# Kernel tuning notes

Hardware: AMD Instinct MI355X
Metric: run time of the kernel (lower is better)

The kernel has to match this reference:

```python
import jax, jax.numpy as jnp
import numpy as np

B, N, F, H, OUT = 64, 512, 128, 256, 6


def setup_inputs() -> dict:
    key = jax.random.key(0)
    ks = jax.random.split(key, 20)
    s = 0.02
    inp = {
        "x": jax.random.normal(ks[0], (B * N, F), dtype=jnp.float32),
        "edge_index": jax.random.randint(ks[1], (2, 16), 0, B * N),
        "edge_weight": jax.random.uniform(ks[2], (16,), dtype=jnp.float32),
        "batch": jnp.repeat(jnp.arange(B, dtype=jnp.int64), N),
        "sigma": jax.random.uniform(ks[3], (1,), dtype=jnp.float32),
        "Wg": s * jax.random.normal(ks[4], (F, F)), "bg": jnp.zeros((F,)),
        "Wrel0": s * jax.random.normal(ks[5], (F, H)), "Wroot0": s * jax.random.normal(ks[6], (F, H)), "brel0": jnp.zeros((H,)),
        "Wrel1": s * jax.random.normal(ks[7], (H, H)), "Wroot1": s * jax.random.normal(ks[8], (H, H)), "brel1": jnp.zeros((H,)),
        "Wrel2": s * jax.random.normal(ks[9], (H, H)), "Wroot2": s * jax.random.normal(ks[10], (H, H)), "brel2": jnp.zeros((H,)),
        "W1": s * jax.random.normal(ks[11], (H, H)), "b1": jnp.zeros((H,)),
        "Wout": s * jax.random.normal(ks[12], (H, OUT)), "bout": jnp.zeros((OUT,)),
    }
    return inp


def _forward(x, sigma, Wg, bg, Wrel0, Wroot0, brel0, Wrel1, Wroot1, brel1,
             Wrel2, Wroot2, brel2, W1, b1, Wout, bout):
    # gdmLinear
    h = x @ Wg + bg                      # [B*N, F]
    hw = h.reshape(B, N, -1)             # to_dense_batch (equal-size windows)
    # pairwise squared distances per window -> Gaussian kernel
    sq = jnp.sum(hw * hw, axis=-1)       # [B, N]
    dist = jnp.maximum(sq[:, :, None] + sq[:, None, :]
                       - 2.0 * jnp.einsum('bnf,bmf->bnm', hw, hw), 0.0)
    A = jnp.exp(-dist / (2.0 * sigma[0] ** 2))   # [B, N, N], all > 0
    A = A * (1.0 - jnp.eye(N, dtype=A.dtype))    # nonzero extraction drops self-loops

    def conv(h, Wrel, Wroot, brel):
        # GraphConv: out_i = W_rel @ sum_j A[j,i] * h_j + b_rel + W_root @ h_i
        agg = jnp.einsum('bji,bjf->bif', A, h)
        return agg @ Wrel + brel + h @ Wroot

    h = hw
    h = jax.nn.relu(conv(h, Wrel0, Wroot0, brel0))
    h = jax.nn.relu(conv(h, Wrel1, Wroot1, brel1))
    h = conv(h, Wrel2, Wroot2, brel2)
    g = jnp.mean(h, axis=1)              # global_mean_pool (equal-size graphs)
    g = jax.nn.relu(g @ W1 + b1)
    return g @ Wout + bout               # [B, OUT]


def reference(x, edge_index, edge_weight, batch, sigma, Wg, bg,
              Wrel0, Wroot0, brel0, Wrel1, Wroot1, brel1,
              Wrel2, Wroot2, brel2, W1, b1, Wout, bout):
    # edge_index / edge_weight / batch inputs are recomputed internally by GdmGNN
    return _forward(x, sigma, Wg, bg, Wrel0, Wroot0, brel0, Wrel1, Wroot1, brel1,
                    Wrel2, Wroot2, brel2, W1, b1, Wout, bout)
```

## Files before the change

kernel.cpp:

```cpp
#include <hip/hip_runtime.h>
#include <math.h>

#define Bsz 64
#define Nn 512
#define Ff 128
#define Hh 256
#define OUTD 6
#define MTOT (Bsz * Nn)

typedef __bf16 bf16x8 __attribute__((ext_vector_type(8)));
typedef float f32x4 __attribute__((ext_vector_type(4)));
typedef int int4v __attribute__((ext_vector_type(4)));
typedef unsigned short ushort4v __attribute__((ext_vector_type(4)));

__device__ __forceinline__ unsigned short f2bf(float f) {
    unsigned u = __float_as_uint(f);
    u += 0x7FFFu + ((u >> 16) & 1u);
    return (unsigned short)(u >> 16);
}
__device__ __forceinline__ float bf2f(unsigned short s) {
    return __uint_as_float(((unsigned)s) << 16);
}

#define SWZ(r) (((r) ^ ((r) >> 2)) & 3)

__device__ __forceinline__ void async_ld16(const unsigned short* g, unsigned short* l) {
    __builtin_amdgcn_global_load_lds(
        (const __attribute__((address_space(1))) void*)g,
        (__attribute__((address_space(3))) void*)l,
        16, 0, 0);
}

#define LDH 40
#define TSZ (128 * 32)

__global__ __launch_bounds__(256) void gemm_bf16(
    const unsigned short* __restrict__ A0, const unsigned short* __restrict__ B0T,
    const unsigned short* __restrict__ A1, const unsigned short* __restrict__ B1T,
    const float* __restrict__ bias,
    unsigned short* __restrict__ C, unsigned short* __restrict__ CT,
    int M, int Ntot, int K0, int K1,
    long strideA0, long strideB0, long strideC, int flags)
{
    int bz = blockIdx.z;
    A0 += (long)bz * strideA0;
    B0T += (long)bz * strideB0;
    C += (long)bz * strideC;

    __shared__ unsigned short As[2 * TSZ];
    __shared__ unsigned short Bs[2 * TSZ];

    int tid = threadIdx.x;
    int lane = tid & 63;
    int wave = tid >> 6;
    int quad = lane >> 4, l16 = lane & 15;
    int wm = (wave >> 1) * 64, wn = (wave & 1) * 64;
    int m0 = blockIdx.x * 128, n0 = blockIdx.y * 128;

    int sr = lane >> 2;
    int sc = lane & 3;

    int T0 = K0 >> 5, T1 = K1 >> 5;
    int T = T0 + T1;

    f32x4 acc[4][4] = {};

    auto issue = [&](int g) {
        const unsigned short* Ag; const unsigned short* Bg; int Kg, kk;
        if (g < T0) { Ag = A0; Bg = B0T; Kg = K0; kk = g << 5; }
        else        { Ag = A1; Bg = B1T; Kg = K1; kk = (g - T0) << 5; }
        unsigned short* Ad = As + (g & 1) * TSZ;
        unsigned short* Bd = Bs + (g & 1) * TSZ;
        #pragma unroll
        for (int t = 0; t < 2; ++t) {
            int r = wave * 32 + t * 16 + sr;
            int c = sc ^ SWZ(r);
            async_ld16(Ag + (long)(m0 + r) * Kg + kk + c * 8,
                       Ad + (wave * 32 + t * 16) * 32);
            async_ld16(Bg + (long)(n0 + r) * Kg + kk + c * 8,
                       Bd + (wave * 32 + t * 16) * 32);
        }
    };

    issue(0);
    for (int g = 0; g < T; ++g) {
        __syncthreads();
        if (g + 1 < T) issue(g + 1);
        const unsigned short* Ab = As + (g & 1) * TSZ;
        const unsigned short* Bb = Bs + (g & 1) * TSZ;
        bf16x8 af[4], bfr[4];
        #pragma unroll
        for (int i = 0; i < 4; ++i) {
            int r = wm + i * 16 + l16;
            af[i] = *(const bf16x8*)&Ab[r * 32 + (quad ^ SWZ(r)) * 8];
        }
        #pragma unroll
        for (int j = 0; j < 4; ++j) {
            int r = wn + j * 16 + l16;
            bfr[j] = *(const bf16x8*)&Bb[r * 32 + (quad ^ SWZ(r)) * 8];
        }
        #pragma unroll
        for (int i = 0; i < 4; ++i)
            #pragma unroll
            for (int j = 0; j < 4; ++j)
                acc[i][j] = __builtin_amdgcn_mfma_f32_16x16x32_bf16(
                    af[i], bfr[j], acc[i][j], 0, 0, 0);
    }

    int ldc = Ntot;
    #pragma unroll
    for (int i = 0; i < 4; ++i) {
        int mb = m0 + wm + i * 16 + quad * 4;
        #pragma unroll
        for (int j = 0; j < 4; ++j) {
            int n = n0 + wn + j * 16 + l16;
            f32x4 v = acc[i][j];
            float bv = bias ? bias[n] : 0.0f;
            float o0 = v[0] + bv, o1 = v[1] + bv, o2 = v[2] + bv, o3 = v[3] + bv;
            if (flags & 1) {
                o0 = fmaxf(o0, 0.f); o1 = fmaxf(o1, 0.f);
                o2 = fmaxf(o2, 0.f); o3 = fmaxf(o3, 0.f);
            }
            unsigned short s0 = f2bf(o0), s1 = f2bf(o1), s2 = f2bf(o2), s3 = f2bf(o3);
            C[(long)(mb + 0) * ldc + n] = s0;
            C[(long)(mb + 1) * ldc + n] = s1;
            C[(long)(mb + 2) * ldc + n] = s2;
            C[(long)(mb + 3) * ldc + n] = s3;
            if (CT) {
                ushort4v p; p[0] = s0; p[1] = s1; p[2] = s2; p[3] = s3;
                long ti = ((long)(mb >> 9) * Ntot + n) * 512 + (mb & 511);
                *(ushort4v*)&CT[ti] = p;
            }
        }
    }
}

__global__ __launch_bounds__(256) void h0_mfma(
    const float* __restrict__ x, const unsigned short* __restrict__ WgT,
    const float* __restrict__ bg,
    unsigned short* __restrict__ h0b, unsigned short* __restrict__ h0T,
    float* __restrict__ sqv)
{
    __shared__ unsigned short As[128 * LDH];
    __shared__ unsigned short Bs[128 * LDH];
    __shared__ float rsq[128];

    int tid = threadIdx.x;
    int lane = tid & 63;
    int wave = tid >> 6;
    int quad = lane >> 4, l16 = lane & 15;
    int wm = (wave >> 1) * 64, wn = (wave & 1) * 64;
    int m0 = blockIdx.x * 128;

    f32x4 acc[4][4] = {};

    for (int k0 = 0; k0 < Ff; k0 += 32) {
        __syncthreads();
        #pragma unroll
        for (int l = 0; l < 2; ++l) {
            int idx = tid + l * 256;
            int r = idx >> 2, ch = idx & 3;
            const float* px = x + (long)(m0 + r) * Ff + k0 + ch * 8;
            float4 xa = *(const float4*)px;
            float4 xb = *(const float4*)(px + 4);
            ushort4v pa, pb;
            pa[0] = f2bf(xa.x); pa[1] = f2bf(xa.y); pa[2] = f2bf(xa.z); pa[3] = f2bf(xa.w);
            pb[0] = f2bf(xb.x); pb[1] = f2bf(xb.y); pb[2] = f2bf(xb.z); pb[3] = f2bf(xb.w);
            *(ushort4v*)&As[r * LDH + ch * 8] = pa;
            *(ushort4v*)&As[r * LDH + ch * 8 + 4] = pb;
            int4v vb = *(const int4v*)(WgT + (long)r * Ff + k0 + ch * 8);
            *(int4v*)&Bs[r * LDH + ch * 8] = vb;
        }
        __syncthreads();
        bf16x8 af[4], bfr[4];
        #pragma unroll
        for (int i = 0; i < 4; ++i)
            af[i] = *(const bf16x8*)&As[(wm + i * 16 + l16) * LDH + quad * 8];
        #pragma unroll
        for (int j = 0; j < 4; ++j)
            bfr[j] = *(const bf16x8*)&Bs[(wn + j * 16 + l16) * LDH + quad * 8];
        #pragma unroll
        for (int i = 0; i < 4; ++i)
            #pragma unroll
            for (int j = 0; j < 4; ++j)
                acc[i][j] = __builtin_amdgcn_mfma_f32_16x16x32_bf16(
                    af[i], bfr[j], acc[i][j], 0, 0, 0);
    }

    if (tid < 128) rsq[tid] = 0.f;
    __syncthreads();

    #pragma unroll
    for (int i = 0; i < 4; ++i) {
        int lrow = wm + i * 16 + quad * 4;
        int mb = m0 + lrow;
        float rp0 = 0.f, rp1 = 0.f, rp2 = 0.f, rp3 = 0.f;
        #pragma unroll
        for (int j = 0; j < 4; ++j) {
            int n = wn + j * 16 + l16;
            f32x4 v = acc[i][j];
            float bv = bg[n];
            unsigned short s0 = f2bf(v[0] + bv), s1 = f2bf(v[1] + bv);
            unsigned short s2 = f2bf(v[2] + bv), s3 = f2bf(v[3] + bv);
            h0b[(long)(mb + 0) * Ff + n] = s0;
            h0b[(long)(mb + 1) * Ff + n] = s1;
            h0b[(long)(mb + 2) * Ff + n] = s2;
            h0b[(long)(mb + 3) * Ff + n] = s3;
            ushort4v p; p[0] = s0; p[1] = s1; p[2] = s2; p[3] = s3;
            long ti = ((long)(mb >> 9) * Ff + n) * 512 + (mb & 511);
            *(ushort4v*)&h0T[ti] = p;
            float f0 = bf2f(s0), f1 = bf2f(s1), f2 = bf2f(s2), f3 = bf2f(s3);
            rp0 += f0 * f0; rp1 += f1 * f1; rp2 += f2 * f2; rp3 += f3 * f3;
        }
        #pragma unroll
        for (int m = 1; m < 16; m <<= 1) {
            rp0 += __shfl_xor(rp0, m);
            rp1 += __shfl_xor(rp1, m);
            rp2 += __shfl_xor(rp2, m);
            rp3 += __shfl_xor(rp3, m);
        }
        if (l16 == 0) {
            atomicAdd(&rsq[lrow + 0], rp0);
            atomicAdd(&rsq[lrow + 1], rp1);
            atomicAdd(&rsq[lrow + 2], rp2);
            atomicAdd(&rsq[lrow + 3], rp3);
        }
    }
    __syncthreads();
    if (tid < 128) sqv[m0 + tid] = rsq[tid];
}

__global__ __launch_bounds__(256) void gram_A_mfma(
    const unsigned short* __restrict__ h0b, const float* __restrict__ sqv,
    const float* __restrict__ sigma, unsigned short* __restrict__ Aout,
    float* __restrict__ w)
{
    int b = blockIdx.z;
    const unsigned short* H = h0b + (long)b * Nn * Ff;
    const float* SQ = sqv + (long)b * Nn;
    unsigned short* Ab = Aout + (long)b * Nn * Nn;

    __shared__ unsigned short Is[2 * TSZ];
    __shared__ unsigned short Js[2 * TSZ];
    __shared__ float rsum[128];

    int tid = threadIdx.x;
    int lane = tid & 63;
    int wave = tid >> 6;
    int quad = lane >> 4, l16 = lane & 15;
    int wm = (wave >> 1) * 64, wn = (wave & 1) * 64;
    int i0 = blockIdx.x * 128, j0 = blockIdx.y * 128;

    int sr = lane >> 2, sc = lane & 3;

    f32x4 acc[4][4] = {};

    auto issue = [&](int g) {
        int kk = g << 5;
        unsigned short* Id = Is + (g & 1) * TSZ;
        unsigned short* Jd = Js + (g & 1) * TSZ;
        #pragma unroll
        for (int t = 0; t < 2; ++t) {
            int r = wave * 32 + t * 16 + sr;
            int c = sc ^ SWZ(r);
            async_ld16(H + (long)(i0 + r) * Ff + kk + c * 8,
                       Id + (wave * 32 + t * 16) * 32);
            async_ld16(H + (long)(j0 + r) * Ff + kk + c * 8,
                       Jd + (wave * 32 + t * 16) * 32);
        }
    };

    issue(0);
    for (int g = 0; g < (Ff >> 5); ++g) {
        __syncthreads();
        if (g + 1 < (Ff >> 5)) issue(g + 1);
        const unsigned short* Ib = Is + (g & 1) * TSZ;
        const unsigned short* Jb = Js + (g & 1) * TSZ;
        bf16x8 af[4], bfr[4];
        #pragma unroll
        for (int i = 0; i < 4; ++i) {
            int r = wm + i * 16 + l16;
            af[i] = *(const bf16x8*)&Ib[r * 32 + (quad ^ SWZ(r)) * 8];
        }
        #pragma unroll
        for (int j = 0; j < 4; ++j) {
            int r = wn + j * 16 + l16;
            bfr[j] = *(const bf16x8*)&Jb[r * 32 + (quad ^ SWZ(r)) * 8];
        }
        #pragma unroll
        for (int i = 0; i < 4; ++i)
            #pragma unroll
            for (int j = 0; j < 4; ++j)
                acc[i][j] = __builtin_amdgcn_mfma_f32_16x16x32_bf16(
                    af[i], bfr[j], acc[i][j], 0, 0, 0);
    }

    if (tid < 128) rsum[tid] = 0.f;
    __syncthreads();

    float s = sigma[0];
    float inv2s2 = 1.0f / (2.0f * s * s);
    #pragma unroll
    for (int i = 0; i < 4; ++i) {
        int lrow = wm + i * 16 + quad * 4;
        int rb = i0 + lrow;
        float rs0 = 0.f, rs1 = 0.f, rs2 = 0.f, rs3 = 0.f;
        #pragma unroll
        for (int j = 0; j < 4; ++j) {
            int c = j0 + wn + j * 16 + l16;
            float sqc = SQ[c];
            f32x4 v = acc[i][j];
            float av[4];
            #pragma unroll
            for (int r4 = 0; r4 < 4; ++r4) {
                int r = rb + r4;
                float d = fmaxf(SQ[r] + sqc - 2.0f * v[r4], 0.0f);
                unsigned short a = (r == c) ? (unsigned short)0
                                            : f2bf(__expf(-d * inv2s2));
                Ab[(long)r * Nn + c] = a;
                av[r4] = bf2f(a);
            }
            rs0 += av[0]; rs1 += av[1]; rs2 += av[2]; rs3 += av[3];
        }
        #pragma unroll
        for (int m = 1; m < 16; m <<= 1) {
            rs0 += __shfl_xor(rs0, m);
            rs1 += __shfl_xor(rs1, m);
            rs2 += __shfl_xor(rs2, m);
            rs3 += __shfl_xor(rs3, m);
        }
        if (l16 == 0) {
            atomicAdd(&rsum[lrow + 0], rs0);
            atomicAdd(&rsum[lrow + 1], rs1);
            atomicAdd(&rsum[lrow + 2], rs2);
            atomicAdd(&rsum[lrow + 3], rs3);
        }
    }
    __syncthreads();
    if (tid < 128) atomicAdd(&w[(long)b * Nn + i0 + tid], rsum[tid]);
}

__global__ __launch_bounds__(256) void convert_weights(
    const float* __restrict__ Wrel0, const float* __restrict__ Wroot0,
    const float* __restrict__ Wrel1, const float* __restrict__ Wroot1,
    const float* __restrict__ Wg,
    unsigned short* __restrict__ T0, unsigned short* __restrict__ T1,
    unsigned short* __restrict__ T2, unsigned short* __restrict__ T3,
    unsigned short* __restrict__ TG,
    float* __restrict__ w, float* __restrict__ vm)
{
    int idx = blockIdx.x * 256 + threadIdx.x;
    if (idx >= 245760) { vm[idx - 245760] = 0.f; return; }
    if (idx >= 212992) { w[idx - 212992] = 0.f; return; }
    if (idx >= 196608) {
        int e = idx - 196608;
        int o = e >> 7, i = e & 127;
        TG[e] = f2bf(Wg[(long)i * 128 + o]);
        return;
    }
    const float* src; unsigned short* dst; int kin; int e;
    if      (idx <  32768) { src = Wrel0;  dst = T0; kin = 128; e = idx; }
    else if (idx <  65536) { src = Wroot0; dst = T1; kin = 128; e = idx - 32768; }
    else if (idx < 131072) { src = Wrel1;  dst = T2; kin = 256; e = idx - 65536; }
    else                   { src = Wroot1; dst = T3; kin = 256; e = idx - 131072; }
    int o = (kin == 128) ? (e >> 7) : (e >> 8);
    int i = e & (kin - 1);
    dst[e] = f2bf(src[(long)i * 256 + o]);
}

__global__ __launch_bounds__(256) void reduce_h2(
    const unsigned short* __restrict__ h2b, const float* __restrict__ w,
    float* __restrict__ v, float* __restrict__ m)
{
    int b = blockIdx.x;
    int jc = blockIdx.y;
    int c = threadIdx.x;
    const unsigned short* H = h2b + ((long)b * Nn + jc * 128) * Hh + c;
    const float* wp = w + (long)b * Nn + jc * 128;
    float vp = 0.f, mp = 0.f;
    #pragma unroll 4
    for (int j = 0; j < 128; ++j) {
        float val = bf2f(H[(long)j * Hh]);
        mp += val;
        vp += wp[j] * val;
    }
    atomicAdd(&v[b * Hh + c], vp);
    atomicAdd(&m[b * Hh + c], mp);
}

__global__ __launch_bounds__(256) void head_kernel(
    const float* __restrict__ v, const float* __restrict__ m,
    const float* __restrict__ Wrel2, const float* __restrict__ Wroot2,
    const float* __restrict__ brel2,
    const float* __restrict__ W1, const float* __restrict__ b1,
    const float* __restrict__ Wout, const float* __restrict__ bout,
    float* __restrict__ out)
{
    int b = blockIdx.x;
    int j = threadIdx.x;
    __shared__ float vs[Hh], ms[Hh], gs[Hh], g2[Hh];
    vs[j] = v[b * Hh + j] * (1.0f / (float)Nn);
    ms[j] = m[b * Hh + j] * (1.0f / (float)Nn);
    __syncthreads();
    float s = brel2[j];
    for (int c = 0; c < Hh; ++c)
        s += vs[c] * Wrel2[c * Hh + j] + ms[c] * Wroot2[c * Hh + j];
    gs[j] = s;
    __syncthreads();
    float t = b1[j];
    for (int k = 0; k < Hh; ++k) t += gs[k] * W1[k * Hh + j];
    g2[j] = fmaxf(t, 0.f);
    __syncthreads();
    if (j < OUTD) {
        float s2 = bout[j];
        for (int k = 0; k < Hh; ++k) s2 += g2[k] * Wout[k * OUTD + j];
        out[b * OUTD + j] = s2;
    }
}

extern "C" void kernel_launch(void* const* d_in, const int* in_sizes, int n_in,
                              void* d_out, int out_size, void* d_ws, size_t ws_size,
                              hipStream_t stream) {
    const float* x      = (const float*)d_in[0];
    const float* sigma  = (const float*)d_in[4];
    const float* Wg     = (const float*)d_in[5];
    const float* bg     = (const float*)d_in[6];
    const float* Wrel0  = (const float*)d_in[7];
    const float* Wroot0 = (const float*)d_in[8];
    const float* brel0  = (const float*)d_in[9];
    const float* Wrel1  = (const float*)d_in[10];
    const float* Wroot1 = (const float*)d_in[11];
    const float* brel1  = (const float*)d_in[12];
    const float* Wrel2  = (const float*)d_in[13];
    const float* Wroot2 = (const float*)d_in[14];
    const float* brel2  = (const float*)d_in[15];
    const float* W1     = (const float*)d_in[16];
    const float* b1     = (const float*)d_in[17];
    const float* Wout   = (const float*)d_in[18];
    const float* bout   = (const float*)d_in[19];
    float* out = (float*)d_out;

    char* ws = (char*)d_ws;
    unsigned short* WgT  = (unsigned short*)(ws + 0);
    unsigned short* h0b  = (unsigned short*)(ws + 16777216);
    unsigned short* h0T  = (unsigned short*)(ws + 25165824);
    float*          sq   = (float*)(ws + 33554432);
    unsigned short* Aadj = (unsigned short*)(ws + 33685504);
    unsigned short* agg  = (unsigned short*)(ws + 67239936);
    unsigned short* h1b  = (unsigned short*)(ws + 84017152);
    unsigned short* h1T  = (unsigned short*)(ws + 100794368);
    unsigned short* h2b  = (unsigned short*)(ws + 117571584);
    unsigned short* WrelT0  = (unsigned short*)(ws + 167903232);
    unsigned short* WrootT0 = (unsigned short*)(ws + 167968768);
    unsigned short* WrelT1  = (unsigned short*)(ws + 168034304);
    unsigned short* WrootT1 = (unsigned short*)(ws + 168165376);
    float*          w    = (float*)(ws + 168558592);
    float*          v    = (float*)(ws + 168689664);
    float*          m    = (float*)(ws + 168755200);

    convert_weights<<<1088, 256, 0, stream>>>(Wrel0, Wroot0, Wrel1, Wroot1, Wg,
                                              WrelT0, WrootT0, WrelT1, WrootT1, WgT,
                                              w, v );

    h0_mfma<<<dim3(MTOT / 128, 1, 1), 256, 0, stream>>>(x, WgT, bg, h0b, h0T, sq);

    gram_A_mfma<<<dim3(Nn / 128, Nn / 128, Bsz), 256, 0, stream>>>(h0b, sq, sigma, Aadj, w);

    gemm_bf16<<<dim3(4, 1, Bsz), 256, 0, stream>>>(
        Aadj, h0T, nullptr, nullptr, nullptr, agg, nullptr,
        Nn, Ff, Nn, 0,
        (long)Nn * Nn, (long)Ff * Nn, (long)Nn * Ff, 0);
    gemm_bf16<<<dim3(MTOT / 128, Hh / 128, 1), 256, 0, stream>>>(
        agg, WrelT0, h0b, WrootT0, brel0, h1b, h1T,
        MTOT, Hh, Ff, Ff, 0, 0, 0, 1);

    gemm_bf16<<<dim3(4, 2, Bsz), 256, 0, stream>>>(
        Aadj, h1T, nullptr, nullptr, nullptr, agg, nullptr,
        Nn, Hh, Nn, 0,
        (long)Nn * Nn, (long)Hh * Nn, (long)Nn * Hh, 0);
    gemm_bf16<<<dim3(MTOT / 128, Hh / 128, 1), 256, 0, stream>>>(
        agg, WrelT1, h1b, WrootT1, brel1, h2b, nullptr,
        MTOT, Hh, Hh, Hh, 0, 0, 0, 1);

    reduce_h2<<<dim3(Bsz, 4), 256, 0, stream>>>(h2b, w, v, m);

    head_kernel<<<Bsz, 256, 0, stream>>>(v, m, Wrel2, Wroot2, brel2,
                                         W1, b1, Wout, bout, out);
}
```

Baseline: 253.9 us.

## Use 512-thread blocks with 8 waves and batch-interleaved block ordering for GEMMs

Doubles the threads per block in the GEMM and Gram kernels to 8 waves. Each wave now computes a 32x64 sub-tile instead of 64x64, which halves accumulator registers and the per-wave load count. The batched GEMM and Gram grids are flattened to 1D with the batch index in the low bits, so consecutive blocks come from different graphs, and reduce_h2 is split into twice as many chunks. The aim is more waves per CU to hide latency and better scheduling across blocks. In exchange each wave has half the MFMA work per LDS read of B fragments, and the epilogue for the Gram kernel must still match the new wave layout.

```diff
diff --git a/kernel.cpp b/kernel.cpp
--- a/kernel.cpp
+++ b/kernel.cpp
@@ -34,7 +34,7 @@
 #define LDH 40
 #define TSZ (128 * 32)
 
-__global__ __launch_bounds__(256) void gemm_bf16(
+__global__ __launch_bounds__(512) void gemm_bf16(
     const unsigned short* __restrict__ A0, const unsigned short* __restrict__ B0T,
     const unsigned short* __restrict__ A1, const unsigned short* __restrict__ B1T,
     const float* __restrict__ bias,
@@ -42,7 +42,15 @@
     int M, int Ntot, int K0, int K1,
     long strideA0, long strideB0, long strideC, int flags)
 {
-    int bz = blockIdx.z;
+    int bx, by, bz;
+    if (flags & 8) {
+        int id = blockIdx.x;
+        bz = id & 63;
+        int t = id >> 6;
+        bx = t & 3;
+        by = t >> 2;
+    } else { bx = blockIdx.x; by = blockIdx.y; bz = blockIdx.z; }
+
     A0 += (long)bz * strideA0;
     B0T += (long)bz * strideB0;
     C += (long)bz * strideC;
@@ -54,8 +62,8 @@
     int lane = tid & 63;
     int wave = tid >> 6;
     int quad = lane >> 4, l16 = lane & 15;
-    int wm = (wave >> 1) * 64, wn = (wave & 1) * 64;
-    int m0 = blockIdx.x * 128, n0 = blockIdx.y * 128;
+    int wm = (wave >> 1) * 32, wn = (wave & 1) * 64;
+    int m0 = bx * 128, n0 = by * 128;
 
     int sr = lane >> 2;
     int sc = lane & 3;
@@ -63,7 +71,7 @@
     int T0 = K0 >> 5, T1 = K1 >> 5;
     int T = T0 + T1;
 
-    f32x4 acc[4][4] = {};
+    f32x4 acc[2][4] = {};
 
     auto issue = [&](int g) {
         const unsigned short* Ag; const unsigned short* Bg; int Kg, kk;
@@ -71,15 +79,10 @@
         else        { Ag = A1; Bg = B1T; Kg = K1; kk = (g - T0) << 5; }
         unsigned short* Ad = As + (g & 1) * TSZ;
         unsigned short* Bd = Bs + (g & 1) * TSZ;
-        #pragma unroll
-        for (int t = 0; t < 2; ++t) {
-            int r = wave * 32 + t * 16 + sr;
-            int c = sc ^ SWZ(r);
-            async_ld16(Ag + (long)(m0 + r) * Kg + kk + c * 8,
-                       Ad + (wave * 32 + t * 16) * 32);
-            async_ld16(Bg + (long)(n0 + r) * Kg + kk + c * 8,
-                       Bd + (wave * 32 + t * 16) * 32);
-        }
+        int r = wave * 16 + sr;
+        int c = sc ^ SWZ(r);
+        async_ld16(Ag + (long)(m0 + r) * Kg + kk + c * 8, Ad + (wave * 16) * 32);
+        async_ld16(Bg + (long)(n0 + r) * Kg + kk + c * 8, Bd + (wave * 16) * 32);
     };
 
     issue(0);
@@ -88,9 +91,9 @@
         if (g + 1 < T) issue(g + 1);
         const unsigned short* Ab = As + (g & 1) * TSZ;
         const unsigned short* Bb = Bs + (g & 1) * TSZ;
-        bf16x8 af[4], bfr[4];
-        #pragma unroll
-        for (int i = 0; i < 4; ++i) {
+        bf16x8 af[2], bfr[4];
+        #pragma unroll
+        for (int i = 0; i < 2; ++i) {
             int r = wm + i * 16 + l16;
             af[i] = *(const bf16x8*)&Ab[r * 32 + (quad ^ SWZ(r)) * 8];
         }
@@ -100,7 +103,7 @@
             bfr[j] = *(const bf16x8*)&Bb[r * 32 + (quad ^ SWZ(r)) * 8];
         }
         #pragma unroll
-        for (int i = 0; i < 4; ++i)
+        for (int i = 0; i < 2; ++i)
             #pragma unroll
             for (int j = 0; j < 4; ++j)
                 acc[i][j] = __builtin_amdgcn_mfma_f32_16x16x32_bf16(
@@ -109,7 +112,7 @@
 
     int ldc = Ntot;
     #pragma unroll
-    for (int i = 0; i < 4; ++i) {
+    for (int i = 0; i < 2; ++i) {
         int mb = m0 + wm + i * 16 + quad * 4;
         #pragma unroll
         for (int j = 0; j < 4; ++j) {
@@ -230,12 +233,16 @@
     if (tid < 128) sqv[m0 + tid] = rsq[tid];
 }
 
-__global__ __launch_bounds__(256) void gram_A_mfma(
+__global__ __launch_bounds__(512) void gram_A_mfma(
     const unsigned short* __restrict__ h0b, const float* __restrict__ sqv,
     const float* __restrict__ sigma, unsigned short* __restrict__ Aout,
     float* __restrict__ w)
 {
-    int b = blockIdx.z;
+    int id = blockIdx.x;
+    int b = id & 63;
+    int t = id >> 6;
+    int i0 = (t & 3) * 128, j0 = (t >> 2) * 128;
+
     const unsigned short* H = h0b + (long)b * Nn * Ff;
     const float* SQ = sqv + (long)b * Nn;
     unsigned short* Ab = Aout + (long)b * Nn * Nn;
@@ -248,26 +255,20 @@
     int lane = tid & 63;
     int wave = tid >> 6;
     int quad = lane >> 4, l16 = lane & 15;
-    int wm = (wave >> 1) * 64, wn = (wave & 1) * 64;
-    int i0 = blockIdx.x * 128, j0 = blockIdx.y * 128;
+    int wm = (wave >> 1) * 32, wn = (wave & 1) * 64;
 
     int sr = lane >> 2, sc = lane & 3;
 
-    f32x4 acc[4][4] = {};
+    f32x4 acc[2][4] = {};
 
     auto issue = [&](int g) {
         int kk = g << 5;
         unsigned short* Id = Is + (g & 1) * TSZ;
         unsigned short* Jd = Js + (g & 1) * TSZ;
-        #pragma unroll
-        for (int t = 0; t < 2; ++t) {
-            int r = wave * 32 + t * 16 + sr;
-            int c = sc ^ SWZ(r);
-            async_ld16(H + (long)(i0 + r) * Ff + kk + c * 8,
-                       Id + (wave * 32 + t * 16) * 32);
-            async_ld16(H + (long)(j0 + r) * Ff + kk + c * 8,
-                       Jd + (wave * 32 + t * 16) * 32);
-        }
+        int r = wave * 16 + sr;
+        int c = sc ^ SWZ(r);
+        async_ld16(H + (long)(i0 + r) * Ff + kk + c * 8, Id + (wave * 16) * 32);
+        async_ld16(H + (long)(j0 + r) * Ff + kk + c * 8, Jd + (wave * 16) * 32);
     };
 
     issue(0);
@@ -276,9 +277,9 @@
         if (g + 1 < (Ff >> 5)) issue(g + 1);
         const unsigned short* Ib = Is + (g & 1) * TSZ;
         const unsigned short* Jb = Js + (g & 1) * TSZ;
-        bf16x8 af[4], bfr[4];
-        #pragma unroll
-        for (int i = 0; i < 4; ++i) {
+        bf16x8 af[2], bfr[4];
+        #pragma unroll
+        for (int i = 0; i < 2; ++i) {
             int r = wm + i * 16 + l16;
             af[i] = *(const bf16x8*)&Ib[r * 32 + (quad ^ SWZ(r)) * 8];
         }
@@ -288,7 +289,7 @@
             bfr[j] = *(const bf16x8*)&Jb[r * 32 + (quad ^ SWZ(r)) * 8];
         }
         #pragma unroll
-        for (int i = 0; i < 4; ++i)
+        for (int i = 0; i < 2; ++i)
             #pragma unroll
             for (int j = 0; j < 4; ++j)
                 acc[i][j] = __builtin_amdgcn_mfma_f32_16x16x32_bf16(
@@ -301,7 +302,7 @@
     float s = sigma[0];
     float inv2s2 = 1.0f / (2.0f * s * s);
     #pragma unroll
-    for (int i = 0; i < 4; ++i) {
+    for (int i = 0; i < 2; ++i) {
         int lrow = wm + i * 16 + quad * 4;
         int rb = i0 + lrow;
         float rs0 = 0.f, rs1 = 0.f, rs2 = 0.f, rs3 = 0.f;
@@ -375,11 +376,11 @@
     int b = blockIdx.x;
     int jc = blockIdx.y;
     int c = threadIdx.x;
-    const unsigned short* H = h2b + ((long)b * Nn + jc * 128) * Hh + c;
-    const float* wp = w + (long)b * Nn + jc * 128;
+    const unsigned short* H = h2b + ((long)b * Nn + jc * 64) * Hh + c;
+    const float* wp = w + (long)b * Nn + jc * 64;
     float vp = 0.f, mp = 0.f;
     #pragma unroll 4
-    for (int j = 0; j < 128; ++j) {
+    for (int j = 0; j < 64; ++j) {
         float val = bf2f(H[(long)j * Hh]);
         mp += val;
         vp += wp[j] * val;
@@ -464,25 +465,25 @@
 
     h0_mfma<<<dim3(MTOT / 128, 1, 1), 256, 0, stream>>>(x, WgT, bg, h0b, h0T, sq);
 
-    gram_A_mfma<<<dim3(Nn / 128, Nn / 128, Bsz), 256, 0, stream>>>(h0b, sq, sigma, Aadj, w);
-
-    gemm_bf16<<<dim3(4, 1, Bsz), 256, 0, stream>>>(
+    gram_A_mfma<<<dim3(16 * Bsz, 1, 1), 512, 0, stream>>>(h0b, sq, sigma, Aadj, w);
+
+    gemm_bf16<<<dim3(4 * Bsz, 1, 1), 512, 0, stream>>>(
         Aadj, h0T, nullptr, nullptr, nullptr, agg, nullptr,
         Nn, Ff, Nn, 0,
-        (long)Nn * Nn, (long)Ff * Nn, (long)Nn * Ff, 0);
-    gemm_bf16<<<dim3(MTOT / 128, Hh / 128, 1), 256, 0, stream>>>(
+        (long)Nn * Nn, (long)Ff * Nn, (long)Nn * Ff, 8);
+    gemm_bf16<<<dim3(MTOT / 128, Hh / 128, 1), 512, 0, stream>>>(
         agg, WrelT0, h0b, WrootT0, brel0, h1b, h1T,
         MTOT, Hh, Ff, Ff, 0, 0, 0, 1);
 
-    gemm_bf16<<<dim3(4, 2, Bsz), 256, 0, stream>>>(
+    gemm_bf16<<<dim3(8 * Bsz, 1, 1), 512, 0, stream>>>(
         Aadj, h1T, nullptr, nullptr, nullptr, agg, nullptr,
         Nn, Hh, Nn, 0,
-        (long)Nn * Nn, (long)Hh * Nn, (long)Nn * Hh, 0);
-    gemm_bf16<<<dim3(MTOT / 128, Hh / 128, 1), 256, 0, stream>>>(
+        (long)Nn * Nn, (long)Hh * Nn, (long)Nn * Hh, 8);
+    gemm_bf16<<<dim3(MTOT / 128, Hh / 128, 1), 512, 0, stream>>>(
         agg, WrelT1, h1b, WrootT1, brel1, h2b, nullptr,
         MTOT, Hh, Hh, Hh, 0, 0, 0, 1);
 
-    reduce_h2<<<dim3(Bsz, 4), 256, 0, stream>>>(h2b, w, v, m);
+    reduce_h2<<<dim3(Bsz, 8), 256, 0, stream>>>(h2b, w, v, m);
 
     head_kernel<<<Bsz, 256, 0, stream>>>(v, m, Wrel2, Wroot2, brel2,
                                          W1, b1, Wout, bout, out);
```

After: 231.7 us. 8.8% less time.
